# Kernel optimization log

Hardware: AMD Instinct MI355X
Metric: run time of the kernel (lower is better)

The kernel has to match this reference:

```python
import jax, jax.numpy as jnp
import numpy as np

N_NODES = 100000
N_EDGES = 1600000
IN_DIM = 3
HID = 128


def setup_inputs() -> dict:
    key = jax.random.key(0)
    ks = jax.random.split(key, 16)
    s = 0.05
    inp = {
        "x": jax.random.normal(ks[0], (N_NODES, IN_DIM), dtype=jnp.float32),
        "pos": jax.random.normal(ks[1], (N_NODES, IN_DIM), dtype=jnp.float32),
        "edge_index": jax.random.randint(ks[2], (2, N_EDGES), 0, N_NODES, dtype=jnp.int64),
        # EdgeConv MLP: Linear(2*IN_DIM, HID) -> ReLU -> Linear(HID, HID)
        "w1": jax.random.normal(ks[3], (2 * IN_DIM, HID), dtype=jnp.float32) * s,
        "b1": jnp.zeros((HID,), dtype=jnp.float32),
        "w2": jax.random.normal(ks[4], (HID, HID), dtype=jnp.float32) * s,
        "b2": jnp.zeros((HID,), dtype=jnp.float32),
        # encoder tail: ReLU -> Linear(HID, HID)
        "w3": jax.random.normal(ks[5], (HID, HID), dtype=jnp.float32) * s,
        "b3": jnp.zeros((HID,), dtype=jnp.float32),
        # decoder: Linear(HID, HID) -> ReLU -> Linear(HID, 3)
        "w4": jax.random.normal(ks[6], (HID, HID), dtype=jnp.float32) * s,
        "b4": jnp.zeros((HID,), dtype=jnp.float32),
        "w5": jax.random.normal(ks[7], (HID, 3), dtype=jnp.float32) * s,
        "b5": jnp.zeros((3,), dtype=jnp.float32),
    }
    return inp


def reference(x, pos, edge_index, w1, b1, w2, b2, w3, b3, w4, b4, w5, b5):
    n = x.shape[0]
    src, dst = edge_index[0], edge_index[1]  # message j(src) -> i(dst)
    xi = x[dst]                               # [E, 3] target features
    xj = x[src]                               # [E, 3] source features
    msg_in = jnp.concatenate([xi, xj - xi], axis=-1)          # [E, 6]
    h = jax.nn.relu(msg_in @ w1 + b1) @ w2 + b2               # [E, HID]
    agg = jax.ops.segment_max(h, dst, num_segments=n)         # [N, HID]
    agg = jnp.where(jnp.isneginf(agg), 0.0, agg)              # nodes with no edges -> 0
    enc = jax.nn.relu(agg) @ w3 + b3                          # [N, HID]
    dec = jax.nn.relu(enc @ w4 + b4) @ w5 + b5                # [N, 3]
    return pos + 0.1 * jnp.tanh(dec)
```

## Files before the change

kernel.cpp:

```cpp
#include <hip/hip_runtime.h>
#include <hip/hip_bf16.h>

typedef __attribute__((ext_vector_type(8))) short short8;
typedef __attribute__((ext_vector_type(4))) float floatx4;
typedef __attribute__((ext_vector_type(2))) unsigned short ushortx2;

#define NHID 128
#define PADROW 136
#define EB 64
#define EB2 128
#define PB 256

__device__ __forceinline__ unsigned short f2bf(float x) {
  unsigned int u = __float_as_uint(x);
  u += 0x7FFFu + ((u >> 16) & 1u);
  return (unsigned short)(u >> 16);
}

__device__ __forceinline__ unsigned int pkbf(float a, float b) {
  __hip_bfloat162 h = __float22bfloat162_rn(make_float2(a, b));
  union { __hip_bfloat162 h; unsigned int u; } cv;
  cv.h = h;
  return cv.u;
}

__device__ __forceinline__ unsigned int pack2(float a, float b) {
  return (unsigned int)f2bf(a) | ((unsigned int)f2bf(b) << 16);
}

__device__ __forceinline__ unsigned int pkmax(unsigned int a, unsigned int b) {
  union { unsigned int u; ushortx2 v; } x, y;
  x.u = a; y.u = b;
  x.v = __builtin_elementwise_max(x.v, y.v);
  return x.u;
}

__device__ __forceinline__ void casmax(unsigned int* ap, unsigned int run) {
  unsigned int old = *ap;
  while (true) {
    unsigned int mx = pkmax(old, run);
    if (mx == old) break;
    unsigned int got = atomicCAS(ap, old, mx);
    if (got == old) break;
    old = got;
  }
}

__device__ __forceinline__ bool detect64(const int* __restrict__ ei) {
  unsigned long long b = __ballot(ei[2 * (threadIdx.x & 63) + 1] != 0);
  return b == 0ULL;
}

__device__ __forceinline__ void load_bfrags(const float* __restrict__ wmat,
                                            short8* bf, int m, int q) {
  #pragma unroll
  for (int kc = 0; kc < 4; ++kc) {
    #pragma unroll
    for (int nt = 0; nt < 8; ++nt) {
      short8 v;
      #pragma unroll
      for (int j = 0; j < 8; ++j)
        v[j] = (short)f2bf(wmat[(kc * 32 + q * 8 + j) * NHID + nt * 16 + m]);
      bf[kc * 8 + nt] = v;
    }
  }
}

__device__ __forceinline__ void load_bfrags_perm(const float* __restrict__ wmat,
                                                 short8* bf, int m, int q) {
  #pragma unroll
  for (int kc = 0; kc < 4; ++kc) {
    #pragma unroll
    for (int nt = 0; nt < 8; ++nt) {
      short8 v;
      #pragma unroll
      for (int j = 0; j < 8; ++j) {
        const int khw = kc * 32 + q * 8 + j;
        const int ctrue = ((khw & 7) << 4) | (khw >> 3);
        v[j] = (short)f2bf(wmat[ctrue * NHID + nt * 16 + m]);
      }
      bf[kc * 8 + nt] = v;
    }
  }
}

__device__ __forceinline__ void mfma_block(const unsigned short* uA,
                                           const short8* bf, floatx4* acc,
                                           int w, int m, int q) {
  #pragma unroll
  for (int kc = 0; kc < 4; ++kc) {
    short8 a = *(const short8*)(uA + (16 * w + m) * PADROW + kc * 32 + q * 8);
    #pragma unroll
    for (int nt = 0; nt < 8; ++nt)
      acc[nt] = __builtin_amdgcn_mfma_f32_16x16x32_bf16(a, bf[kc * 8 + nt],
                                                        acc[nt], 0, 0, 0);
  }
}

__global__ void zero_detect_kernel(float4* __restrict__ p, int n4,
                                   const int* __restrict__ ei, int* __restrict__ flag) {
  if (blockIdx.x == 0 && threadIdx.x < 64) {
    unsigned long long b = __ballot(ei[2 * threadIdx.x + 1] != 0);
    if (threadIdx.x == 0) flag[0] = (b == 0ULL) ? 1 : 0;
  }
  int i = blockIdx.x * blockDim.x + threadIdx.x;
  int stride = gridDim.x * blockDim.x;
  float4 z = make_float4(0.f, 0.f, 0.f, 0.f);
  for (; i < n4; i += stride) p[i] = z;
}


__global__ __launch_bounds__(256) void part_hist(const int* __restrict__ ei,
                                                 int* __restrict__ mat, int E, int nbuck,
                                                 float4* __restrict__ aggz, int n4) {
  const int bl = blockIdx.x, t = threadIdx.x;
  if (bl >= PB) {
    int i = (bl - PB) * 256 + t;
    const int st = (gridDim.x - PB) * 256;
    float4 z = make_float4(0.f, 0.f, 0.f, 0.f);
    for (; i < n4; i += st) aggz[i] = z;
    return;
  }
  __shared__ int hist[512];
  const bool is64 = detect64(ei);
  for (int i = t; i < nbuck; i += 256) hist[i] = 0;
  __syncthreads();
  const int chunk = (E + PB - 1) / PB;
  const int lo = bl * chunk;
  const int hi = min(lo + chunk, E);
  for (int i = lo + t; i < hi; i += 256) {
    int d = is64 ? ei[2 * E + 2 * i] : ei[E + i];
    atomicAdd(&hist[d >> 8], 1);
  }
  __syncthreads();
  for (int bu = t; bu < nbuck; bu += 256) mat[bu * PB + bl] = hist[bu];
}

__global__ __launch_bounds__(256) void scan_rows(int* __restrict__ mat,
                                                 int* __restrict__ btot, int nbuck) {
  __shared__ int sh[256];
  const int bu = blockIdx.x, t = threadIdx.x;
  const int v = mat[bu * PB + t];
  sh[t] = v;
  __syncthreads();
  for (int off = 1; off < 256; off <<= 1) {
    int x = (t >= off) ? sh[t - off] : 0;
    __syncthreads();
    sh[t] += x;
    __syncthreads();
  }
  mat[bu * PB + t] = sh[t] - v;
  if (t == 255) btot[bu] = sh[255];
}

__global__ __launch_bounds__(256) void part_scatter(const int* __restrict__ ei,
                                                    const int* __restrict__ mat,
                                                    const int* __restrict__ btot,
                                                    int* __restrict__ bstart,
                                                    int2* __restrict__ mid, int E, int nbuck) {
  __shared__ int off[512];
  __shared__ int bsS[512];
  const bool is64 = detect64(ei);
  const int bl = blockIdx.x, t = threadIdx.x;
  const int o0 = (t < nbuck) ? btot[t] : 0;
  const int o1 = (t + 256 < nbuck) ? btot[t + 256] : 0;
  bsS[t] = o0; bsS[t + 256] = o1;
  __syncthreads();
  for (int o = 1; o < 256; o <<= 1) {
    int x0 = (t >= o) ? bsS[t - o] : 0;
    int x1 = (t >= o) ? bsS[256 + t - o] : 0;
    __syncthreads();
    bsS[t] += x0; bsS[256 + t] += x1;
    __syncthreads();
  }
  const int tot0 = bsS[255];
  bsS[256 + t] += tot0;
  __syncthreads();
  const int ex0 = bsS[t] - o0;
  const int ex1 = bsS[256 + t] - o1;
  if (bl == 0) { bstart[t] = ex0; bstart[256 + t] = ex1; }
  off[t]       = ex0 + ((t < nbuck) ? mat[t * PB + bl] : 0);
  off[256 + t] = ex1 + ((t + 256 < nbuck) ? mat[(t + 256) * PB + bl] : 0);
  __syncthreads();
  const int chunk = (E + PB - 1) / PB;
  const int lo = bl * chunk;
  const int hi = min(lo + chunk, E);
  for (int i = lo + t; i < hi; i += 256) {
    int s = is64 ? ei[2 * i]         : ei[i];
    int d = is64 ? ei[2 * E + 2 * i] : ei[E + i];
    int p = atomicAdd(&off[d >> 8], 1);
    mid[p] = make_int2(s, d);
  }
}

__global__ __launch_bounds__(256) void bucket_sort(const int2* __restrict__ mid,
                                                   const int* __restrict__ bstart,
                                                   int2* __restrict__ sorted) {
  __shared__ int h[256], cnt[256];
  const int bu = blockIdx.x, t = threadIdx.x;
  const int lo = bstart[bu], hi = bstart[bu + 1];
  h[t] = 0; cnt[t] = 0;
  __syncthreads();
  for (int i = lo + t; i < hi; i += 256) atomicAdd(&h[mid[i].y & 255], 1);
  __syncthreads();
  const int v = h[t];
  for (int off = 1; off < 256; off <<= 1) {
    int x = (t >= off) ? h[t - off] : 0;
    __syncthreads();
    h[t] += x;
    __syncthreads();
  }
  const int excl = h[t] - v;
  __syncthreads();
  h[t] = excl;
  __syncthreads();
  for (int i = lo + t; i < hi; i += 256) {
    int2 e = mid[i];
    const int dl = e.y & 255;
    const int p = lo + h[dl] + atomicAdd(&cnt[dl], 1);
    sorted[p] = e;
  }
}


__global__ __launch_bounds__(512, 2) void edge_sorted_kernel(
    const float* __restrict__ x, const int2* __restrict__ sorted,
    const float* __restrict__ w1, const float* __restrict__ b1,
    const float* __restrict__ w2, const float* __restrict__ b2,
    unsigned int* aggu, int N, int E) {
  __shared__ unsigned short us[EB2 * PADROW];
  __shared__ short8 w2f[2048];
  __shared__ int esS[EB2], edS[EB2];
  __shared__ int pn[2];
  __shared__ unsigned long long maskS[2];
  __shared__ unsigned int pmS[8][64];

  const int t = threadIdx.x;
  const int lane = t & 63;
  const int w = t >> 6;
  const int m = lane & 15;
  const int q = lane >> 4;

  float b1c[8], b2c[8];
  #pragma unroll
  for (int nt = 0; nt < 8; ++nt) { b1c[nt] = b1[nt * 16 + m]; b2c[nt] = b2[nt * 16 + m]; }

  short8 bf1[8];
  #pragma unroll
  for (int nt = 0; nt < 8; ++nt) {
    short8 v;
    #pragma unroll
    for (int j = 0; j < 8; ++j)
      v[j] = (q == 0 && j < 6) ? (short)f2bf(w1[j * NHID + nt * 16 + m]) : (short)0;
    bf1[nt] = v;
  }

  for (int idx = t; idx < 2048; idx += 512) {
    const int fg = idx >> 6, ln = idx & 63;
    const int mm = ln & 15;
    const int kc = fg >> 3, nt = fg & 7;
    short8 v;
    #pragma unroll
    for (int j = 0; j < 8; ++j) {
      const int khw = kc * 32 + (ln >> 4) * 8 + j;
      const int ctrue = ((khw & 7) << 4) | (khw >> 3);
      v[j] = (short)f2bf(w2[ctrue * NHID + nt * 16 + mm]);
    }
    w2f[idx] = v;
  }

  const int jc = t & 63;
  const int quarter = t >> 6;

  const int nbt = (E + EB2 - 1) / EB2;
  __syncthreads();

  int2 sv = make_int2(0, -1);
  {
    const int tile0 = blockIdx.x;
    const int gb = tile0 * EB2;
    if (t < EB2) {
      const int e = gb + t;
      if (tile0 < nbt && e < E) sv = sorted[e];
    } else if (t == EB2) {
      sv.y = (tile0 < nbt && gb > 0) ? sorted[gb - 1].y : -2;
    } else if (t == EB2 + 1) {
      sv.y = (tile0 < nbt && gb + EB2 < E) ? sorted[gb + EB2].y : -2;
    }
  }

  for (int tile = blockIdx.x; tile < nbt; tile += gridDim.x) {
    if (t < EB2) { esS[t] = sv.x; edS[t] = sv.y; }
    else if (t == EB2) pn[0] = sv.y;
    else if (t == EB2 + 1) pn[1] = sv.y;
    __syncthreads();

    if (w == 0) {
      int d0 = edS[lane];
      int dp0 = (lane == 0) ? -9 : edS[lane - 1];
      unsigned long long mk0 = __ballot(lane == 0 || d0 != dp0);
      int d1 = edS[64 + lane];
      int dp1 = edS[63 + lane];
      unsigned long long mk1 = __ballot(d1 != dp1);
      if (lane == 0) { maskS[0] = mk0; maskS[1] = mk1; }
    }

    floatx4 acc[8];
    #pragma unroll
    for (int nt = 0; nt < 8; ++nt) { floatx4 z = {0.f, 0.f, 0.f, 0.f}; acc[nt] = z; }
    short8 a1 = {0, 0, 0, 0, 0, 0, 0, 0};
    if (q == 0) {
      const int e = 16 * w + m;
      const int si = esS[e];
      const int d0 = edS[e];
      const int di = (d0 < 0) ? 0 : d0;
      float xi0 = x[di * 3], xi1 = x[di * 3 + 1], xi2 = x[di * 3 + 2];
      float dd0 = x[si * 3] - xi0, dd1 = x[si * 3 + 1] - xi1, dd2 = x[si * 3 + 2] - xi2;
      union { short8 s; uint4 u; } cv;
      cv.u = make_uint4(pkbf(xi0, xi1), pkbf(xi2, dd0), pkbf(dd1, dd2), 0u);
      a1 = cv.s;
    }
    #pragma unroll
    for (int nt = 0; nt < 8; ++nt)
      acc[nt] = __builtin_amdgcn_mfma_f32_16x16x32_bf16(a1, bf1[nt], acc[nt], 0, 0, 0);

    #pragma unroll
    for (int r = 0; r < 4; ++r) {
      union { short8 s; uint4 u; } cv;
      cv.u = make_uint4(
        pkbf(fmaxf(acc[0][r] + b1c[0], 0.f), fmaxf(acc[1][r] + b1c[1], 0.f)),
        pkbf(fmaxf(acc[2][r] + b1c[2], 0.f), fmaxf(acc[3][r] + b1c[3], 0.f)),
        pkbf(fmaxf(acc[4][r] + b1c[4], 0.f), fmaxf(acc[5][r] + b1c[5], 0.f)),
        pkbf(fmaxf(acc[6][r] + b1c[6], 0.f), fmaxf(acc[7][r] + b1c[7], 0.f)));
      *(short8*)(&us[(16 * w + q * 4 + r) * PADROW + m * 8]) = cv.s;
    }
    __syncthreads();

    #pragma unroll
    for (int nt = 0; nt < 8; ++nt) { floatx4 z = {0.f, 0.f, 0.f, 0.f}; acc[nt] = z; }
    #pragma unroll
    for (int kc = 0; kc < 4; ++kc) {
      short8 a = *(const short8*)(&us[(16 * w + m) * PADROW + kc * 32 + q * 8]);
      #pragma unroll
      for (int nt = 0; nt < 8; ++nt)
        acc[nt] = __builtin_amdgcn_mfma_f32_16x16x32_bf16(a, w2f[(kc * 8 + nt) * 64 + lane],
                                                          acc[nt], 0, 0, 0);
    }
    __syncthreads();

    #pragma unroll
    for (int r = 0; r < 4; ++r) {
      union { short8 s; uint4 u; } cv;
      cv.u = make_uint4(
        pkbf(fmaxf(acc[0][r] + b2c[0], 0.f), fmaxf(acc[1][r] + b2c[1], 0.f)),
        pkbf(fmaxf(acc[2][r] + b2c[2], 0.f), fmaxf(acc[3][r] + b2c[3], 0.f)),
        pkbf(fmaxf(acc[4][r] + b2c[4], 0.f), fmaxf(acc[5][r] + b2c[5], 0.f)),
        pkbf(fmaxf(acc[6][r] + b2c[6], 0.f), fmaxf(acc[7][r] + b2c[7], 0.f)));
      *(short8*)(&us[(16 * w + q * 4 + r) * PADROW + m * 8]) = cv.s;
    }
    __syncthreads();

    {
      const int tn = tile + gridDim.x;
      const int gb = tn * EB2;
      int2 nv = make_int2(0, -1);
      if (t < EB2) {
        const int e = gb + t;
        if (tn < nbt && e < E) nv = sorted[e];
      } else if (t == EB2) {
        nv.y = (tn < nbt && gb > 0) ? sorted[gb - 1].y : -2;
      } else if (t == EB2 + 1) {
        nv.y = (tn < nbt && gb + EB2 < E) ? sorted[gb + EB2].y : -2;
      }
      sv = nv;
    }

    int os = -1, onxt = 0, od = -1; unsigned int opart = 0;
    {
      const unsigned long long mk0 = maskS[0], mk1 = maskS[1];
      const int prevd = pn[0], nextd = pn[1];
      const int r0 = quarter * 16, r1 = r0 + 16;
      const unsigned int* us32 = (const unsigned int*)us;
      int s;
      if (r0 < 64) {
        s = 63 - __builtin_clzll(mk0 & (~0ULL >> (63 - r0)));
      } else {
        unsigned long long hm = mk1 & (~0ULL >> (127 - r0));
        s = hm ? 127 - __builtin_clzll(hm) : 63 - __builtin_clzll(mk0);
      }
      while (s < r1) {
        int nxt;
        if (s < 63) {
          unsigned long long ab = mk0 & (~0ULL << (s + 1));
          if (ab) nxt = __builtin_ffsll((long long)ab) - 1;
          else    nxt = mk1 ? 64 + __builtin_ffsll((long long)mk1) - 1 : 128;
        } else if (s == 63) {
          nxt = mk1 ? 64 + __builtin_ffsll((long long)mk1) - 1 : 128;
        } else if (s < 127) {
          unsigned long long ab = mk1 & (~0ULL << (s - 63));
          nxt = ab ? 64 + __builtin_ffsll((long long)ab) - 1 : 128;
        } else nxt = 128;

        const int lo = (s > r0) ? s : r0;
        const int hi = (nxt < r1) ? nxt : r1;
        unsigned int run = 0;
        for (int r = lo; r < hi; ++r)
          run = pkmax(run, us32[r * (PADROW >> 1) + jc]);

        if (s < r0) {
          pmS[quarter][jc] = run;
        } else if (nxt <= r1) {
          const int d = edS[s];
          if (d >= 0) {
            const bool bnd = (s == 0 && prevd == d) || (nxt == 128 && nextd == d);
            unsigned int* ap = aggu + (size_t)d * 64 + jc;
            if (!bnd) *ap = run;
            else if (run) casmax(ap, run);
          }
        } else {
          os = s; onxt = nxt; od = edS[s]; opart = run;
        }
        s = nxt;
      }
    }
    __syncthreads();

    if (os >= 0 && od >= 0) {
      const int endq = (onxt - 1) >> 4;
      #pragma unroll 4
      for (int qq = quarter + 1; qq <= endq; ++qq)
        opart = pkmax(opart, pmS[qq][jc]);
      const bool bnd = (os == 0 && pn[0] == od) || (onxt == 128 && pn[1] == od);
      unsigned int* ap = aggu + (size_t)od * 64 + jc;
      if (!bnd) *ap = opart;
      else if (opart) casmax(ap, opart);
    }
    __syncthreads();
  }
}


__global__ __launch_bounds__(256, 2) void edge_atomic_kernel(
    const float* __restrict__ x, const int* __restrict__ ei,
    const float* __restrict__ w1, const float* __restrict__ b1,
    const float* __restrict__ w2, const float* __restrict__ b2,
    unsigned int* aggu, const int* __restrict__ flag64, int N, int E) {
  __shared__ unsigned short uA[EB * PADROW];
  __shared__ float w1s[6 * NHID];
  __shared__ float b1s[NHID], b2s[NHID];
  __shared__ int es[EB], ed[EB];

  const int t = threadIdx.x;
  const int lane = t & 63;
  const int w = t >> 6;
  const int m = lane & 15;
  const int q = lane >> 4;

  for (int i = t; i < 6 * NHID; i += 256) w1s[i] = w1[i];
  if (t < NHID) { b1s[t] = b1[t]; b2s[t] = b2[t]; }

  short8 bf[32];
  load_bfrags(w2, bf, m, q);

  const bool is64 = (flag64[0] != 0);
  const int nb = (E + EB - 1) / EB;

  for (int batch = blockIdx.x; batch < nb; batch += gridDim.x) {
    const int gbase = batch * EB;
    if (t < EB) {
      int e = gbase + t;
      es[t] = (e < E) ? (is64 ? ei[2 * e] : ei[e]) : 0;
    } else if (t < 2 * EB) {
      int tt = t - EB;
      int e = gbase + tt;
      ed[tt] = (e < E) ? (is64 ? ei[2 * E + 2 * e] : ei[E + e]) : 0;
    }
    __syncthreads();
    {
      const int e = t >> 2;
      const int c0 = (t & 3) * 32;
      const int si = es[e], di = ed[e];
      float xi0 = x[di * 3], xi1 = x[di * 3 + 1], xi2 = x[di * 3 + 2];
      float msg[6];
      msg[0] = xi0; msg[1] = xi1; msg[2] = xi2;
      msg[3] = x[si * 3] - xi0; msg[4] = x[si * 3 + 1] - xi1; msg[5] = x[si * 3 + 2] - xi2;
      unsigned int* d32 = (unsigned int*)uA;
      const int base32 = (e * PADROW + c0) >> 1;
      #pragma unroll
      for (int cc = 0; cc < 32; cc += 2) {
        float u0 = b1s[c0 + cc], u1 = b1s[c0 + cc + 1];
        #pragma unroll
        for (int d = 0; d < 6; ++d) {
          u0 += msg[d] * w1s[d * NHID + c0 + cc];
          u1 += msg[d] * w1s[d * NHID + c0 + cc + 1];
        }
        d32[base32 + (cc >> 1)] = pack2(fmaxf(u0, 0.f), fmaxf(u1, 0.f));
      }
    }
    __syncthreads();

    floatx4 acc[8];
    #pragma unroll
    for (int nt = 0; nt < 8; ++nt) { floatx4 z = {0.f, 0.f, 0.f, 0.f}; acc[nt] = z; }
    mfma_block(uA, bf, acc, w, m, q);

    #pragma unroll
    for (int nt = 0; nt < 8; ++nt) {
      const int c = nt * 16 + m;
      const float bb = b2s[c];
      const int kst = m * 8 + nt;
      #pragma unroll
      for (int r = 0; r < 4; ++r) {
        const int erow = 16 * w + q * 4 + r;
        if (gbase + erow < E) {
          float hb = acc[nt][r] + bb;
          if (hb > 0.f) {
            unsigned int v = (unsigned int)f2bf(hb);
            casmax(aggu + (size_t)ed[erow] * 64 + (kst >> 1), v << (16 * (kst & 1)));
          }
        }
      }
    }
    __syncthreads();
  }
}


__global__ __launch_bounds__(256, 2) void encdec_kernel(
    const float* __restrict__ w3, const float* __restrict__ b3,
    const float* __restrict__ w4, const float* __restrict__ b4,
    const float* __restrict__ w5, const float* __restrict__ b5,
    const float* __restrict__ pos, const unsigned short* __restrict__ agg16,
    float* __restrict__ out, int N) {
  __shared__ unsigned short uA[EB * PADROW];
  __shared__ short8 w4f[2048];
  __shared__ float w5s[NHID * 3];

  const int t = threadIdx.x;
  const int lane = t & 63;
  const int w = t >> 6;
  const int m = lane & 15;
  const int q = lane >> 4;

  float b3c[8], b4c[8];
  #pragma unroll
  for (int nt = 0; nt < 8; ++nt) { b3c[nt] = b3[nt * 16 + m]; b4c[nt] = b4[nt * 16 + m]; }

  short8 bf3[32];
  load_bfrags_perm(w3, bf3, m, q);

  for (int idx = t; idx < 2048; idx += 256) {
    const int fg = idx >> 6, ln = idx & 63;
    const int mm = ln & 15;
    const int kc = fg >> 3, nt = fg & 7;
    short8 v;
    #pragma unroll
    for (int j = 0; j < 8; ++j) {
      const int khw = kc * 32 + (ln >> 4) * 8 + j;
      const int ctrue = ((khw & 7) << 4) | (khw >> 3);
      v[j] = (short)f2bf(w4[ctrue * NHID + nt * 16 + mm]);
    }
    w4f[idx] = v;
  }
  for (int i = t; i < NHID * 3; i += 256) w5s[i] = w5[i];
  const float b50 = b5[0], b51 = b5[1], b52 = b5[2];

  const int ch = t & 15;
  const int rr = t >> 4;
  const int nb = (N + EB - 1) / EB;
  __syncthreads();

  uint4 rv[4];
  const uint4 uz = make_uint4(0u, 0u, 0u, 0u);
  {
    const int b0 = blockIdx.x;
    #pragma unroll
    for (int k = 0; k < 4; ++k) {
      const int node = b0 * EB + rr + 16 * k;
      rv[k] = (b0 < nb && node < N) ? ((const uint4*)agg16)[(size_t)node * 16 + ch] : uz;
    }
  }

  for (int batch = blockIdx.x; batch < nb; batch += gridDim.x) {
    const int base = batch * EB;
    #pragma unroll
    for (int k = 0; k < 4; ++k)
      *(uint4*)(&uA[(rr + 16 * k) * PADROW + ch * 8]) = rv[k];
    __syncthreads();

    {
      const int nxb = batch + gridDim.x;
      #pragma unroll
      for (int k = 0; k < 4; ++k) {
        const int node = nxb * EB + rr + 16 * k;
        rv[k] = (nxb < nb && node < N) ? ((const uint4*)agg16)[(size_t)node * 16 + ch] : uz;
      }
    }

    floatx4 acc[8];
    #pragma unroll
    for (int nt = 0; nt < 8; ++nt) { floatx4 z = {0.f, 0.f, 0.f, 0.f}; acc[nt] = z; }
    mfma_block(uA, bf3, acc, w, m, q);
    __syncthreads();

    #pragma unroll
    for (int r = 0; r < 4; ++r) {
      union { short8 s; uint4 u; } cv;
      cv.u = make_uint4(
        pkbf(acc[0][r] + b3c[0], acc[1][r] + b3c[1]),
        pkbf(acc[2][r] + b3c[2], acc[3][r] + b3c[3]),
        pkbf(acc[4][r] + b3c[4], acc[5][r] + b3c[5]),
        pkbf(acc[6][r] + b3c[6], acc[7][r] + b3c[7]));
      *(short8*)(&uA[(16 * w + q * 4 + r) * PADROW + m * 8]) = cv.s;
    }
    __syncthreads();

    #pragma unroll
    for (int nt = 0; nt < 8; ++nt) { floatx4 z = {0.f, 0.f, 0.f, 0.f}; acc[nt] = z; }
    #pragma unroll
    for (int kc = 0; kc < 4; ++kc) {
      short8 a = *(const short8*)(&uA[(16 * w + m) * PADROW + kc * 32 + q * 8]);
      #pragma unroll
      for (int nt = 0; nt < 8; ++nt)
        acc[nt] = __builtin_amdgcn_mfma_f32_16x16x32_bf16(a, w4f[(kc * 8 + nt) * 64 + lane],
                                                          acc[nt], 0, 0, 0);
    }

    float p[4][3];
    #pragma unroll
    for (int r = 0; r < 4; ++r) { p[r][0] = 0.f; p[r][1] = 0.f; p[r][2] = 0.f; }
    #pragma unroll
    for (int nt = 0; nt < 8; ++nt) {
      const int c = nt * 16 + m;
      const float bb = b4c[nt];
      const float w50 = w5s[c * 3], w51 = w5s[c * 3 + 1], w52 = w5s[c * 3 + 2];
      #pragma unroll
      for (int r = 0; r < 4; ++r) {
        float tv = fmaxf(acc[nt][r] + bb, 0.f);
        p[r][0] += tv * w50; p[r][1] += tv * w51; p[r][2] += tv * w52;
      }
    }
    #pragma unroll
    for (int off = 8; off >= 1; off >>= 1) {
      #pragma unroll
      for (int r = 0; r < 4; ++r) {
        p[r][0] += __shfl_xor(p[r][0], off, 16);
        p[r][1] += __shfl_xor(p[r][1], off, 16);
        p[r][2] += __shfl_xor(p[r][2], off, 16);
      }
    }
    if (m == 0) {
      #pragma unroll
      for (int r = 0; r < 4; ++r) {
        const int node = base + 16 * w + q * 4 + r;
        if (node < N) {
          out[node * 3]     = pos[node * 3]     + 0.1f * tanhf(p[r][0] + b50);
          out[node * 3 + 1] = pos[node * 3 + 1] + 0.1f * tanhf(p[r][1] + b51);
          out[node * 3 + 2] = pos[node * 3 + 2] + 0.1f * tanhf(p[r][2] + b52);
        }
      }
    }
    __syncthreads();
  }
}

extern "C" void kernel_launch(void* const* d_in, const int* in_sizes, int n_in,
                              void* d_out, int out_size, void* d_ws, size_t ws_size,
                              hipStream_t stream) {
  const float* x   = (const float*)d_in[0];
  const float* pos = (const float*)d_in[1];
  const int*   ei  = (const int*)d_in[2];
  const float* w1  = (const float*)d_in[3];
  const float* b1  = (const float*)d_in[4];
  const float* w2  = (const float*)d_in[5];
  const float* b2  = (const float*)d_in[6];
  const float* w3  = (const float*)d_in[7];
  const float* b3  = (const float*)d_in[8];
  const float* w4  = (const float*)d_in[9];
  const float* b4  = (const float*)d_in[10];
  const float* w5  = (const float*)d_in[11];
  const float* b5  = (const float*)d_in[12];
  float* out = (float*)d_out;

  const int N = in_sizes[0] / 3;
  const int E = in_sizes[2] / 2;
  const int nbuck = (N + 255) >> 8;

  char* ws = (char*)d_ws;
  unsigned short* agg16 = (unsigned short*)ws;
  const size_t aggB = (size_t)N * NHID * sizeof(unsigned short);
  int2* mid    = (int2*)(ws + aggB);
  int2* sorted = (int2*)(ws + aggB + (size_t)E * 8);
  int*  mat    = (int*)(ws + aggB + (size_t)E * 16);
  int*  btot   = mat + (size_t)nbuck * PB;
  int*  bstart = btot + nbuck;
  const size_t needed = aggB + (size_t)E * 16 + ((size_t)nbuck * PB + nbuck + 520) * 4;

  if (ws_size >= needed && nbuck <= 511 && E >= 64) {
    part_hist<<<2048, 256, 0, stream>>>(ei, mat, E, nbuck, (float4*)agg16, N * 16);
    scan_rows<<<nbuck, 256, 0, stream>>>(mat, btot, nbuck);
    part_scatter<<<PB, 256, 0, stream>>>(ei, mat, btot, bstart, mid, E, nbuck);
    bucket_sort<<<nbuck, 256, 0, stream>>>(mid, bstart, sorted);
    edge_sorted_kernel<<<512, 512, 0, stream>>>(x, sorted, w1, b1, w2, b2,
                                                (unsigned int*)agg16, N, E);
  } else {
    int* flag2 = (int*)(ws + aggB);
    zero_detect_kernel<<<2048, 256, 0, stream>>>((float4*)agg16, N * 16, ei, flag2);
    edge_atomic_kernel<<<512, 256, 0, stream>>>(x, ei, w1, b1, w2, b2,
                                                (unsigned int*)agg16, flag2, N, E);
  }
  encdec_kernel<<<512, 256, 0, stream>>>(w3, b3, w4, b4, w5, b5, pos, agg16, out, N);
}
```

Before: 348.9 us.

## Fuse four sort-phase kernels into one persistent kernel with grid barriers

The histogram, row-scan, scatter and bucket-sort kernels are merged into one 256-block kernel that separates the phases with an atomic-counter global barrier, and the aggregate zeroing is folded into the first phase. This removes three kernel launches and the gaps between them, at the cost of a memset for the counter. It relies on all 256 blocks being co-resident, otherwise it deadlocks. The zeroing now runs on 256 blocks instead of 1792 extra ones, and the per-bucket phases loop over buckets on fewer blocks.

```diff
diff --git a/kernel.cpp b/kernel.cpp
--- a/kernel.cpp
+++ b/kernel.cpp
@@ -51,6 +51,17 @@
   return b == 0ULL;
 }
 
+__device__ __forceinline__ void gbar(unsigned int* cnt, unsigned int target) {
+  __threadfence();
+  __syncthreads();
+  if (threadIdx.x == 0) {
+    atomicAdd(cnt, 1u);
+    while (atomicAdd(cnt, 0u) < target) __builtin_amdgcn_s_sleep(2);
+  }
+  __syncthreads();
+  __threadfence();
+}
+
 __device__ __forceinline__ void load_bfrags(const float* __restrict__ wmat,
                                             short8* bf, int m, int q) {
   #pragma unroll
@@ -110,115 +121,103 @@
 }
 
 
-__global__ __launch_bounds__(256) void part_hist(const int* __restrict__ ei,
-                                                 int* __restrict__ mat, int E, int nbuck,
-                                                 float4* __restrict__ aggz, int n4) {
+__global__ __launch_bounds__(256) void sort_fused(
+    const int* __restrict__ ei, int E, int nbuck,
+    int* __restrict__ mat, int* __restrict__ btot, int* __restrict__ bstart,
+    int2* __restrict__ mid, int2* __restrict__ sorted,
+    float4* __restrict__ aggz, int n4, unsigned int* __restrict__ cnt) {
+  __shared__ int shA[512];
+  __shared__ int shB[512];
   const int bl = blockIdx.x, t = threadIdx.x;
-  if (bl >= PB) {
-    int i = (bl - PB) * 256 + t;
-    const int st = (gridDim.x - PB) * 256;
-    float4 z = make_float4(0.f, 0.f, 0.f, 0.f);
-    for (; i < n4; i += st) aggz[i] = z;
-    return;
-  }
-  __shared__ int hist[512];
   const bool is64 = detect64(ei);
-  for (int i = t; i < nbuck; i += 256) hist[i] = 0;
-  __syncthreads();
   const int chunk = (E + PB - 1) / PB;
   const int lo = bl * chunk;
   const int hi = min(lo + chunk, E);
+
+  for (int i = t; i < nbuck; i += 256) shA[i] = 0;
+  __syncthreads();
   for (int i = lo + t; i < hi; i += 256) {
     int d = is64 ? ei[2 * E + 2 * i] : ei[E + i];
-    atomicAdd(&hist[d >> 8], 1);
+    atomicAdd(&shA[d >> 8], 1);
+  }
+  {
+    float4 z = make_float4(0.f, 0.f, 0.f, 0.f);
+    for (int i = bl * 256 + t; i < n4; i += PB * 256) aggz[i] = z;
   }
   __syncthreads();
-  for (int bu = t; bu < nbuck; bu += 256) mat[bu * PB + bl] = hist[bu];
-}
-
-__global__ __launch_bounds__(256) void scan_rows(int* __restrict__ mat,
-                                                 int* __restrict__ btot, int nbuck) {
-  __shared__ int sh[256];
-  const int bu = blockIdx.x, t = threadIdx.x;
-  const int v = mat[bu * PB + t];
-  sh[t] = v;
-  __syncthreads();
-  for (int off = 1; off < 256; off <<= 1) {
-    int x = (t >= off) ? sh[t - off] : 0;
-    __syncthreads();
-    sh[t] += x;
-    __syncthreads();
-  }
-  mat[bu * PB + t] = sh[t] - v;
-  if (t == 255) btot[bu] = sh[255];
-}
-
-__global__ __launch_bounds__(256) void part_scatter(const int* __restrict__ ei,
-                                                    const int* __restrict__ mat,
-                                                    const int* __restrict__ btot,
-                                                    int* __restrict__ bstart,
-                                                    int2* __restrict__ mid, int E, int nbuck) {
-  __shared__ int off[512];
-  __shared__ int bsS[512];
-  const bool is64 = detect64(ei);
-  const int bl = blockIdx.x, t = threadIdx.x;
-  const int o0 = (t < nbuck) ? btot[t] : 0;
-  const int o1 = (t + 256 < nbuck) ? btot[t + 256] : 0;
-  bsS[t] = o0; bsS[t + 256] = o1;
-  __syncthreads();
-  for (int o = 1; o < 256; o <<= 1) {
-    int x0 = (t >= o) ? bsS[t - o] : 0;
-    int x1 = (t >= o) ? bsS[256 + t - o] : 0;
-    __syncthreads();
-    bsS[t] += x0; bsS[256 + t] += x1;
-    __syncthreads();
-  }
-  const int tot0 = bsS[255];
-  bsS[256 + t] += tot0;
-  __syncthreads();
-  const int ex0 = bsS[t] - o0;
-  const int ex1 = bsS[256 + t] - o1;
-  if (bl == 0) { bstart[t] = ex0; bstart[256 + t] = ex1; }
-  off[t]       = ex0 + ((t < nbuck) ? mat[t * PB + bl] : 0);
-  off[256 + t] = ex1 + ((t + 256 < nbuck) ? mat[(t + 256) * PB + bl] : 0);
-  __syncthreads();
-  const int chunk = (E + PB - 1) / PB;
-  const int lo = bl * chunk;
-  const int hi = min(lo + chunk, E);
-  for (int i = lo + t; i < hi; i += 256) {
-    int s = is64 ? ei[2 * i]         : ei[i];
-    int d = is64 ? ei[2 * E + 2 * i] : ei[E + i];
-    int p = atomicAdd(&off[d >> 8], 1);
-    mid[p] = make_int2(s, d);
-  }
-}
-
-__global__ __launch_bounds__(256) void bucket_sort(const int2* __restrict__ mid,
-                                                   const int* __restrict__ bstart,
-                                                   int2* __restrict__ sorted) {
-  __shared__ int h[256], cnt[256];
-  const int bu = blockIdx.x, t = threadIdx.x;
-  const int lo = bstart[bu], hi = bstart[bu + 1];
-  h[t] = 0; cnt[t] = 0;
-  __syncthreads();
-  for (int i = lo + t; i < hi; i += 256) atomicAdd(&h[mid[i].y & 255], 1);
-  __syncthreads();
-  const int v = h[t];
-  for (int off = 1; off < 256; off <<= 1) {
-    int x = (t >= off) ? h[t - off] : 0;
-    __syncthreads();
-    h[t] += x;
-    __syncthreads();
-  }
-  const int excl = h[t] - v;
-  __syncthreads();
-  h[t] = excl;
-  __syncthreads();
-  for (int i = lo + t; i < hi; i += 256) {
-    int2 e = mid[i];
-    const int dl = e.y & 255;
-    const int p = lo + h[dl] + atomicAdd(&cnt[dl], 1);
-    sorted[p] = e;
+  for (int bu = t; bu < nbuck; bu += 256) mat[bu * PB + bl] = shA[bu];
+  gbar(cnt, PB * 1);
+
+  for (int bu = bl; bu < nbuck; bu += PB) {
+    const int v = mat[bu * PB + t];
+    shA[t] = v;
+    __syncthreads();
+    for (int off = 1; off < 256; off <<= 1) {
+      int x = (t >= off) ? shA[t - off] : 0;
+      __syncthreads();
+      shA[t] += x;
+      __syncthreads();
+    }
+    mat[bu * PB + t] = shA[t] - v;
+    if (t == 255) btot[bu] = shA[255];
+    __syncthreads();
+  }
+  gbar(cnt, PB * 2);
+
+  {
+    const int o0 = (t < nbuck) ? btot[t] : 0;
+    const int o1 = (t + 256 < nbuck) ? btot[t + 256] : 0;
+    shA[t] = o0; shA[t + 256] = o1;
+    __syncthreads();
+    for (int o = 1; o < 256; o <<= 1) {
+      int x0 = (t >= o) ? shA[t - o] : 0;
+      int x1 = (t >= o) ? shA[256 + t - o] : 0;
+      __syncthreads();
+      shA[t] += x0; shA[256 + t] += x1;
+      __syncthreads();
+    }
+    const int tot0 = shA[255];
+    shA[256 + t] += tot0;
+    __syncthreads();
+    const int ex0 = shA[t] - o0;
+    const int ex1 = shA[256 + t] - o1;
+    if (bl == 0) { bstart[t] = ex0; bstart[256 + t] = ex1; }
+    shB[t]       = ex0 + ((t < nbuck) ? mat[t * PB + bl] : 0);
+    shB[256 + t] = ex1 + ((t + 256 < nbuck) ? mat[(t + 256) * PB + bl] : 0);
+    __syncthreads();
+    for (int i = lo + t; i < hi; i += 256) {
+      int s = is64 ? ei[2 * i]         : ei[i];
+      int d = is64 ? ei[2 * E + 2 * i] : ei[E + i];
+      int p = atomicAdd(&shB[d >> 8], 1);
+      mid[p] = make_int2(s, d);
+    }
+  }
+  gbar(cnt, PB * 3);
+
+  for (int bu = bl; bu < nbuck; bu += PB) {
+    const int blo = bstart[bu], bhi = bstart[bu + 1];
+    shA[t] = 0; shB[t] = 0;
+    __syncthreads();
+    for (int i = blo + t; i < bhi; i += 256) atomicAdd(&shA[mid[i].y & 255], 1);
+    __syncthreads();
+    const int v = shA[t];
+    for (int off = 1; off < 256; off <<= 1) {
+      int x = (t >= off) ? shA[t - off] : 0;
+      __syncthreads();
+      shA[t] += x;
+      __syncthreads();
+    }
+    const int excl = shA[t] - v;
+    __syncthreads();
+    shA[t] = excl;
+    __syncthreads();
+    for (int i = blo + t; i < bhi; i += 256) {
+      int2 e = mid[i];
+      const int dl = e.y & 255;
+      const int p = blo + shA[dl] + atomicAdd(&shB[dl], 1);
+      sorted[p] = e;
+    }
+    __syncthreads();
   }
 }
 
@@ -694,13 +693,13 @@
   int*  mat    = (int*)(ws + aggB + (size_t)E * 16);
   int*  btot   = mat + (size_t)nbuck * PB;
   int*  bstart = btot + nbuck;
-  const size_t needed = aggB + (size_t)E * 16 + ((size_t)nbuck * PB + nbuck + 520) * 4;
+  unsigned int* cnt = (unsigned int*)(bstart + 513);
+  const size_t needed = aggB + (size_t)E * 16 + ((size_t)nbuck * PB + nbuck + 513 + 8) * 4;
 
   if (ws_size >= needed && nbuck <= 511 && E >= 64) {
-    part_hist<<<2048, 256, 0, stream>>>(ei, mat, E, nbuck, (float4*)agg16, N * 16);
-    scan_rows<<<nbuck, 256, 0, stream>>>(mat, btot, nbuck);
-    part_scatter<<<PB, 256, 0, stream>>>(ei, mat, btot, bstart, mid, E, nbuck);
-    bucket_sort<<<nbuck, 256, 0, stream>>>(mid, bstart, sorted);
+    hipMemsetAsync(cnt, 0, sizeof(unsigned int), stream);
+    sort_fused<<<PB, 256, 0, stream>>>(ei, E, nbuck, mat, btot, bstart,
+                                       mid, sorted, (float4*)agg16, N * 16, cnt);
     edge_sorted_kernel<<<512, 512, 0, stream>>>(x, sorted, w1, b1, w2, b2,
                                                 (unsigned int*)agg16, N, E);
   } else {
```

Measured after the change: 520.6 us. 49.2% more time.
